# Optimization experiments

Hardware: AMD Instinct MI355X
Metric: run time of the kernel (lower is better)

Reference implementation:

```python
import jax, jax.numpy as jnp
import numpy as np

HEADS = 4

def _dwconv(x, w, pad):
    # depthwise conv, NCHW, kernel [C,1,k,k]
    return jax.lax.conv_general_dilated(
        x, w, window_strides=(1, 1), padding=((pad, pad), (pad, pad)),
        feature_group_count=x.shape[1],
        dimension_numbers=('NCHW', 'OIHW', 'NCHW'))

def _l2norm(t):
    # matches torch F.normalize(dim=-1, eps=1e-12)
    n = jnp.sqrt(jnp.sum(t * t, axis=-1, keepdims=True))
    return t / jnp.maximum(n, 1e-12)

def _reshape_attn(q, k, v, temp, if_box):
    b, c, hw0 = q.shape
    factor = HEADS
    ch = c // HEADS
    pad = (-hw0) % factor

    def prep(t):
        t = jnp.pad(t, ((0, 0), (0, 0), (0, pad)))
        hw = t.shape[-1] // factor
        if if_box:  # 'b (head c) (factor hw) -> b head (c factor) hw'
            t = t.reshape(b, HEADS, ch, factor, hw)
        else:       # 'b (head c) (hw factor) -> b head (c factor) hw'
            t = t.reshape(b, HEADS, ch, hw, factor).transpose(0, 1, 2, 4, 3)
        return t.reshape(b, HEADS, ch * factor, hw)

    qq, kk, vv = prep(q), prep(k), prep(v)
    qq, kk = _l2norm(qq), _l2norm(kk)
    attn = jnp.einsum('bhdn,bhen->bhde', qq, kk) * temp  # temp [heads,1,1]
    e = jnp.exp(attn)
    attn = e / (jnp.sum(e, axis=-1, keepdims=True) + 1.0)  # softmax_1
    o = jnp.einsum('bhde,bhen->bhdn', attn, vv)
    hw = o.shape[-1]
    if if_box:
        o = o.reshape(b, HEADS, ch, factor, hw).reshape(b, c, factor * hw)
    else:
        o = o.reshape(b, HEADS, ch, factor, hw).transpose(0, 1, 2, 4, 3).reshape(b, c, hw * factor)
    return o[:, :, :hw0]

def _conv1x1(x, w):
    return jnp.einsum('bchw,oc->bohw', x, w)

def _forward(x, temperature, w_qkv, w_dw3, w_dw5, w_dw7, w_fuse, b_fuse, w_proj):
    b, c, h, w = x.shape
    ch = c // 2
    # sort first half of channels along h then w
    xh = x[:, :ch]
    idx_h = jnp.argsort(xh, axis=-2)
    xs = jnp.take_along_axis(xh, idx_h, axis=-2)
    idx_w = jnp.argsort(xs, axis=-1)
    xs = jnp.take_along_axis(xs, idx_w, axis=-1)
    x = jnp.concatenate([xs, x[:, ch:]], axis=1)

    q = _conv1x1(x, w_qkv)  # [b,5c,h,w]
    cat = jnp.concatenate([_dwconv(q, w_dw3, 1), _dwconv(q, w_dw5, 2), _dwconv(q, w_dw7, 3)], axis=1)
    qkv = _conv1x1(cat, w_fuse) + b_fuse[None, :, None, None]
    q1, k1, q2, k2, v = jnp.split(qkv, 5, axis=1)

    hw = h * w
    vf = v.reshape(b, c, hw)
    idx = jnp.argsort(vf, axis=-1)
    vs = jnp.take_along_axis(vf, idx, axis=-1)
    gat = lambda t: jnp.take_along_axis(t.reshape(b, c, hw), idx, axis=-1)

    out1 = _reshape_attn(gat(q1), gat(k1), vs, temperature, True)
    out2 = _reshape_attn(gat(q2), gat(k2), vs, temperature, False)

    inv = jnp.argsort(idx, axis=-1)  # scatter(out, 2, idx, out) == unsort
    out1 = jnp.take_along_axis(out1, inv, axis=-1).reshape(b, c, h, w)
    out2 = jnp.take_along_axis(out2, inv, axis=-1).reshape(b, c, h, w)

    out = _conv1x1(out1 * out2, w_proj)
    r = out[:, :ch]
    r = jnp.take_along_axis(r, jnp.argsort(idx_w, axis=-1), axis=-1)
    r = jnp.take_along_axis(r, jnp.argsort(idx_h, axis=-2), axis=-2)
    return jnp.concatenate([r, out[:, ch:]], axis=1)

def setup_inputs() -> dict:
    key = jax.random.key(0)
    ks = jax.random.split(key, 8)
    b, c, h, w = 2, 64, 192, 192
    x = jax.random.normal(ks[0], (b, c, h, w), jnp.float32)
    temperature = jnp.ones((HEADS, 1, 1), jnp.float32)
    w_qkv = jax.random.normal(ks[1], (5 * c, c), jnp.float32) * 0.05
    w_dw3 = jax.random.normal(ks[2], (5 * c, 1, 3, 3), jnp.float32) * 0.1
    w_dw5 = jax.random.normal(ks[3], (5 * c, 1, 5, 5), jnp.float32) * 0.05
    w_dw7 = jax.random.normal(ks[4], (5 * c, 1, 7, 7), jnp.float32) * 0.03
    w_fuse = jax.random.normal(ks[5], (5 * c, 15 * c), jnp.float32) * 0.02
    b_fuse = jnp.zeros((5 * c,), jnp.float32)
    w_proj = jax.random.normal(ks[6], (c, c), jnp.float32) * 0.05
    return {'x': x, 'temperature': temperature, 'w_qkv': w_qkv, 'w_dw3': w_dw3,
            'w_dw5': w_dw5, 'w_dw7': w_dw7, 'w_fuse': w_fuse, 'b_fuse': b_fuse,
            'w_proj': w_proj}

def reference(x, temperature, w_qkv, w_dw3, w_dw5, w_dw7, w_fuse, b_fuse, w_proj):
    return _forward(x, temperature, w_qkv, w_dw3, w_dw5, w_dw7, w_fuse, b_fuse, w_proj)
```

## Files before the change

### kernel.cpp

```cpp
#include <hip/hip_runtime.h>
#include <stdint.h>
#include <stddef.h>

constexpr int IMH = 192;
constexpr int IMW = 192;
constexpr int HW  = 36864;
constexpr int BB  = 2;
constexpr int CC  = 64;
constexpr int CHF = 32;
constexpr int C5  = 320;
constexpr int NQ  = 9216;
constexpr int CROWS = 64;
constexpr int CHWN  = CROWS * IMW;
constexpr int NCHUNK = 32;
constexpr int CHN = HW / 4 / NCHUNK;
constexpr int NSEG = 12;
constexpr int SEGN = HW / NSEG;
constexpr int NBIN = 2048;

typedef float fx2 __attribute__((ext_vector_type(2)));
typedef float fx4 __attribute__((ext_vector_type(4)));
typedef _Float16 f16;
typedef _Float16 f16x8 __attribute__((ext_vector_type(8)));
typedef float f32x4 __attribute__((ext_vector_type(4)));

static __device__ __forceinline__ uint32_t f2s(float f) {
    uint32_t u = __float_as_uint(f);
    return (u & 0x80000000u) ? ~u : (u | 0x80000000u);
}
static __device__ __forceinline__ float s2f(uint32_t s) {
    uint32_t u = (s & 0x80000000u) ? (s & 0x7FFFFFFFu) : ~s;
    return __uint_as_float(u);
}

static __device__ void bitonic256(uint64_t* keys, int tid) {
    for (unsigned k = 2; k <= 256; k <<= 1) {
        for (unsigned j = k >> 1; j; j >>= 1) {
            __syncthreads();
            unsigned i = ((tid & ~(j - 1)) << 1) | (tid & (j - 1));
            unsigned p = i | j;
            bool up = ((i & k) == 0);
            uint64_t a = keys[i], b = keys[p];
            if ((a > b) == up) { keys[i] = b; keys[p] = a; }
        }
    }
    __syncthreads();
}

__global__ __launch_bounds__(128) void k_sort_h(const float* __restrict__ x, float* __restrict__ A,
                                                int* __restrict__ idx_h) {
    __shared__ uint64_t keys[256];
    int tid = threadIdx.x;
    int blk = blockIdx.x;
    int w = blk % IMW;
    int c = (blk / IMW) % CHF;
    int b = blk / (IMW * CHF);
    const float* col = x + ((size_t)(b * CC) + c) * HW + w;
    for (int i = tid; i < 256; i += 128)
        keys[i] = (i < IMH) ? ((((uint64_t)f2s(col[(size_t)i * IMW])) << 32) | (uint32_t)i) : ~0ull;
    bitonic256(keys, tid);
    float* ocol = A + ((size_t)(b * CC) + c) * HW + w;
    int* icol = idx_h + ((size_t)(b * CHF) + c) * HW + w;
    for (int i = tid; i < IMH; i += 128) {
        uint64_t k = keys[i];
        ocol[(size_t)i * IMW] = s2f((uint32_t)(k >> 32));
        icol[(size_t)i * IMW] = (int)(k & 0xFFFFFFFFull);
    }
}

__global__ __launch_bounds__(128) void k_sort_w(float* __restrict__ A, int* __restrict__ idx_w) {
    __shared__ uint64_t keys[256];
    int tid = threadIdx.x;
    int blk = blockIdx.x;
    int h = blk % IMH;
    int c = (blk / IMH) % CHF;
    int b = blk / (IMH * CHF);
    float* row = A + ((size_t)(b * CC) + c) * HW + (size_t)h * IMW;
    for (int i = tid; i < 256; i += 128)
        keys[i] = (i < IMW) ? ((((uint64_t)f2s(row[i])) << 32) | (uint32_t)i) : ~0ull;
    bitonic256(keys, tid);
    int* irow = idx_w + ((size_t)(b * CHF) + c) * HW + (size_t)h * IMW;
    for (int i = tid; i < IMW; i += 128) {
        uint64_t k = keys[i];
        row[i] = s2f((uint32_t)(k >> 32));
        irow[i] = (int)(k & 0xFFFFFFFFull);
    }
}

__global__ __launch_bounds__(256) void k_gemm_q(const float* __restrict__ wq, const float* __restrict__ A,
                                                const float* __restrict__ x, float* __restrict__ q) {
    __shared__ float Wt[64][68];
    __shared__ float Xt[64][68];
    int tid = threadIdx.x;
    int n0 = blockIdx.x * 64, m0 = blockIdx.y * 64, b = blockIdx.z;
    for (int l = 0; l < 16; ++l) {
        int idx = l * 256 + tid;
        int cc = idx & 63, m = idx >> 6;
        Wt[cc][m] = wq[(size_t)(m0 + m) * 64 + cc];
    }
    for (int l = 0; l < 16; ++l) {
        int idx = l * 256 + tid;
        int n = idx & 63, cc = idx >> 6;
        const float* sp = (cc < CHF) ? A : x;
        Xt[cc][n] = sp[((size_t)(b * CC) + cc) * HW + n0 + n];
    }
    __syncthreads();
    int ty = tid >> 4, tx = tid & 15;
    float acc[4][4] = {};
    for (int cc = 0; cc < 64; ++cc) {
        float4 av = *(const float4*)&Wt[cc][ty * 4];
        float4 bv = *(const float4*)&Xt[cc][tx * 4];
        float aa[4] = {av.x, av.y, av.z, av.w};
        float bb[4] = {bv.x, bv.y, bv.z, bv.w};
        #pragma unroll
        for (int i = 0; i < 4; ++i)
            #pragma unroll
            for (int j = 0; j < 4; ++j)
                acc[i][j] = fmaf(aa[i], bb[j], acc[i][j]);
    }
    for (int i = 0; i < 4; ++i) {
        float4 o;
        o.x = acc[i][0]; o.y = acc[i][1]; o.z = acc[i][2]; o.w = acc[i][3];
        *(float4*)&q[((size_t)(b * C5) + m0 + ty * 4 + i) * HW + n0 + tx * 4] = o;
    }
}

template <int KS>
__global__ __launch_bounds__(256) void k_dwconv(const float* __restrict__ q, const float* __restrict__ wd,
                                                float* __restrict__ slice, int r0) {
    constexpr int PAD = KS / 2;
    constexpr int EXT = 32 + 2 * PAD;
    __shared__ float tile[EXT][EXT];
    int tid = threadIdx.x;
    int b = blockIdx.z, c = blockIdx.y;
    int t = blockIdx.x;
    int ty0 = r0 + (t / 6) * 32, tx0 = (t % 6) * 32;
    const float* src = q + ((size_t)(b * C5) + c) * HW;
    for (int i = tid; i < EXT * EXT; i += 256) {
        int iy = i / EXT, ix = i % EXT;
        int gy = ty0 + iy - PAD, gx = tx0 + ix - PAD;
        float v = 0.f;
        if (gy >= 0 && gy < IMH && gx >= 0 && gx < IMW) v = src[gy * IMW + gx];
        tile[iy][ix] = v;
    }
    __syncthreads();
    float wreg[KS * KS];
    #pragma unroll
    for (int i = 0; i < KS * KS; ++i) wreg[i] = wd[(size_t)c * KS * KS + i];
    float* dst = slice + ((size_t)(b * C5) + c) * CHWN;
    #pragma unroll
    for (int k = 0; k < 4; ++k) {
        int pix = k * 256 + tid;
        int py = pix >> 5, px = pix & 31;
        float acc = 0.f;
        #pragma unroll
        for (int ky = 0; ky < KS; ++ky)
            #pragma unroll
            for (int kx = 0; kx < KS; ++kx)
                acc = fmaf(tile[py + ky][px + kx], wreg[ky * KS + kx], acc);
        dst[(ty0 - r0 + py) * IMW + tx0 + px] = acc;
    }
}

__global__ __launch_bounds__(256) void k_gemm_fuse(const float* __restrict__ wf,
                                                   const float* __restrict__ slice, const float* __restrict__ bias,
                                                   float* __restrict__ qkv, int g, int r0) {
    __shared__ f16 Ah[64][40];
    __shared__ f16 Al[64][40];
    int tid = threadIdx.x;
    int n0 = blockIdx.x * 128, m0 = blockIdx.y * 64, b = blockIdx.z;
    int lane = tid & 63, wv = tid >> 6;
    int l15 = lane & 15, lg = lane >> 4;
    int nwave = n0 + wv * 32;
    int sm = tid >> 2, skr = (tid & 3) * 8;
    int gk = g * 320;
    f32x4 acc[4][2];
    #pragma unroll
    for (int i = 0; i < 4; ++i)
        #pragma unroll
        for (int j = 0; j < 2; ++j)
            acc[i][j] = (f32x4){0.f, 0.f, 0.f, 0.f};

    const float* xcol = slice + (size_t)(b * C5) * CHWN + nwave + l15;
    const float* wrow = wf + (size_t)(m0 + sm) * 960 + gk + skr;

    for (int k0 = 0; k0 < 320; k0 += 32) {
        if (k0) __syncthreads();
        {
            float4 w0 = *(const float4*)(wrow + k0);
            float4 w1 = *(const float4*)(wrow + k0 + 4);
            float wvv[8] = {w0.x, w0.y, w0.z, w0.w, w1.x, w1.y, w1.z, w1.w};
            f16x8 hv, lv;
            #pragma unroll
            for (int j = 0; j < 8; ++j) {
                f16 h = (f16)wvv[j];
                hv[j] = h;
                lv[j] = (f16)(wvv[j] - (float)h);
            }
            *(f16x8*)&Ah[sm][skr] = hv;
            *(f16x8*)&Al[sm][skr] = lv;
        }
        float xv[2][8];
        #pragma unroll
        for (int fn = 0; fn < 2; ++fn)
            #pragma unroll
            for (int j = 0; j < 8; ++j)
                xv[fn][j] = xcol[(size_t)(k0 + lg * 8 + j) * CHWN + fn * 16];
        __syncthreads();
        f16x8 bh[2], bl[2];
        #pragma unroll
        for (int fn = 0; fn < 2; ++fn)
            #pragma unroll
            for (int j = 0; j < 8; ++j) {
                float v = xv[fn][j];
                f16 h = (f16)v;
                bh[fn][j] = h;
                bl[fn][j] = (f16)(v - (float)h);
            }
        #pragma unroll
        for (int fm = 0; fm < 4; ++fm) {
            f16x8 ah = *(const f16x8*)&Ah[fm * 16 + l15][lg * 8];
            f16x8 al = *(const f16x8*)&Al[fm * 16 + l15][lg * 8];
            #pragma unroll
            for (int fn = 0; fn < 2; ++fn) {
                acc[fm][fn] = __builtin_amdgcn_mfma_f32_16x16x32_f16(ah, bh[fn], acc[fm][fn], 0, 0, 0);
                acc[fm][fn] = __builtin_amdgcn_mfma_f32_16x16x32_f16(ah, bl[fn], acc[fm][fn], 0, 0, 0);
                acc[fm][fn] = __builtin_amdgcn_mfma_f32_16x16x32_f16(al, bh[fn], acc[fm][fn], 0, 0, 0);
            }
        }
    }

    #pragma unroll
    for (int fm = 0; fm < 4; ++fm) {
        #pragma unroll
        for (int r = 0; r < 4; ++r) {
            int m = m0 + fm * 16 + lg * 4 + r;
            size_t base = ((size_t)(b * C5) + m) * HW + (size_t)r0 * IMW;
            if (g == 0) {
                float bv = bias[m];
                #pragma unroll
                for (int fn = 0; fn < 2; ++fn)
                    qkv[base + nwave + fn * 16 + l15] = acc[fm][fn][r] + bv;
            } else {
                #pragma unroll
                for (int fn = 0; fn < 2; ++fn)
                    qkv[base + nwave + fn * 16 + l15] += acc[fm][fn][r];
            }
        }
    }
}

template <int FIRST>
__global__ __launch_bounds__(256) void k_rcount(const uint64_t* __restrict__ in, const float* __restrict__ qkvv,
                                                uint32_t* __restrict__ cntG, int shift) {
    __shared__ uint32_t hist[NBIN];
    int t = threadIdx.x;
    int seg = blockIdx.x, row = blockIdx.y;
    #pragma unroll
    for (int k = 0; k < NBIN / 256; ++k) hist[k * 256 + t] = 0;
    __syncthreads();
    if (FIRST) {
        int bb = row >> 6, c = row & 63;
        const float* srcf = qkvv + ((size_t)(bb * C5) + 256 + c) * HW + (size_t)seg * SEGN;
        #pragma unroll
        for (int i = 0; i < SEGN / 256; ++i) {
            unsigned d = f2s(srcf[i * 256 + t]) & (NBIN - 1);
            atomicAdd(&hist[d], 1u);
        }
    } else {
        const uint64_t* src = in + (size_t)row * HW + (size_t)seg * SEGN;
        #pragma unroll
        for (int i = 0; i < SEGN / 256; ++i) {
            unsigned d = (unsigned)(src[i * 256 + t] >> shift) & (NBIN - 1);
            atomicAdd(&hist[d], 1u);
        }
    }
    __syncthreads();
    uint32_t* dstc = cntG + ((size_t)row * NSEG + seg) * NBIN;
    #pragma unroll
    for (int k = 0; k < NBIN / 256; ++k) dstc[k * 256 + t] = hist[k * 256 + t];
}

__global__ __launch_bounds__(256) void k_rscan(uint32_t* __restrict__ cntG) {
    __shared__ uint32_t tot[NBIN];
    __shared__ uint32_t gsum[256];
    __shared__ uint32_t gbase[256];
    int t = threadIdx.x;
    int row = blockIdx.x;
    uint32_t* base = cntG + (size_t)row * NSEG * NBIN;
    uint32_t loc = 0;
    #pragma unroll
    for (int k = 0; k < NBIN / 256; ++k) {
        int bn = t * (NBIN / 256) + k;
        uint32_t s = 0;
        for (int sg = 0; sg < NSEG; ++sg) s += base[sg * NBIN + bn];
        tot[bn] = s;
        loc += s;
    }
    gsum[t] = loc;
    __syncthreads();
    if (t == 0) {
        uint32_t acc = 0;
        for (int i = 0; i < 256; ++i) { uint32_t v = gsum[i]; gbase[i] = acc; acc += v; }
    }
    __syncthreads();
    uint32_t run = gbase[t];
    #pragma unroll
    for (int k = 0; k < NBIN / 256; ++k) {
        int bn = t * (NBIN / 256) + k;
        uint32_t tv = tot[bn];
        uint32_t r2 = run;
        for (int sg = 0; sg < NSEG; ++sg) {
            uint32_t cv = base[sg * NBIN + bn];
            base[sg * NBIN + bn] = r2;
            r2 += cv;
        }
        run += tv;
    }
}

template <int MODE>
__global__ __launch_bounds__(256) void k_rscatter(const uint64_t* __restrict__ in, const float* __restrict__ qkvv,
                                                  uint64_t* __restrict__ out, float* __restrict__ vso,
                                                  int* __restrict__ idxo, int* __restrict__ inv0o,
                                                  int* __restrict__ inv1o, const uint32_t* __restrict__ cntG,
                                                  int shift) {
    __shared__ uint16_t wcnt[4][NBIN];
    __shared__ uint32_t runbase[NBIN];
    int t = threadIdx.x;
    int w = t >> 6, lane = t & 63;
    int seg = blockIdx.x, row = blockIdx.y;
    const uint32_t* cbase = cntG + ((size_t)row * NSEG + seg) * NBIN;
    #pragma unroll
    for (int k = 0; k < NBIN / 256; ++k) runbase[k * 256 + t] = cbase[k * 256 + t];
    for (int i = 0; i < SEGN / 256; ++i) {
        __syncthreads();
        #pragma unroll
        for (int k = 0; k < NBIN / 256; ++k)
            ((uint64_t*)wcnt)[k * 256 + t] = 0;
        __syncthreads();
        uint64_t kv;
        if (MODE == 1) {
            int bb = row >> 6, c = row & 63;
            const float* srcf = qkvv + ((size_t)(bb * C5) + 256 + c) * HW + (size_t)seg * SEGN;
            kv = (((uint64_t)f2s(srcf[i * 256 + t])) << 32) | (uint32_t)(seg * SEGN + i * 256 + t);
        } else {
            const uint64_t* src = in + (size_t)row * HW + (size_t)seg * SEGN;
            kv = src[i * 256 + t];
        }
        unsigned d = (unsigned)(kv >> shift) & (NBIN - 1);
        uint64_t peers = ~0ull;
        #pragma unroll
        for (int bit = 0; bit < 11; ++bit) {
            uint64_t bm = __ballot((d >> bit) & 1u);
            peers &= ((d >> bit) & 1u) ? bm : ~bm;
        }
        unsigned lanerank = (unsigned)__popcll(peers & ((1ull << lane) - 1ull));
        unsigned wtotal = (unsigned)__popcll(peers);
        if (lanerank == 0) wcnt[w][d] = (uint16_t)wtotal;
        __syncthreads();
        unsigned wpre = 0;
        #pragma unroll
        for (int ww = 0; ww < 4; ++ww) {
            unsigned cv = wcnt[ww][d];
            if (ww < w) wpre += cv;
        }
        unsigned pos = runbase[d] + wpre + lanerank;
        if (MODE == 2) {
            int j = (int)(kv & 0xFFFFFFFFull);
            vso[(size_t)row * HW + pos] = s2f((uint32_t)(kv >> 32));
            idxo[(size_t)row * HW + pos] = j;
            int bb = row >> 6, c = row & 63;
            int* ip = (bb ? inv1o : inv0o) + (size_t)c * HW;
            ip[j] = (int)pos;
        } else {
            out[(size_t)row * HW + pos] = kv;
        }
        __syncthreads();
        #pragma unroll
        for (int k = 0; k < NBIN / 256; ++k) {
            int bn = k * 256 + t;
            runbase[bn] += (uint32_t)wcnt[0][bn] + wcnt[1][bn] + wcnt[2][bn] + wcnt[3][bn];
        }
    }
}

__global__ __launch_bounds__(1024) void k_scatter4(const int* __restrict__ inv0, const int* __restrict__ inv1,
                                                   const float* __restrict__ qkv, float* __restrict__ g4) {
    int i = blockIdx.x;
    int row = (i & 7) * 16 + ((i >> 3) & 15);
    int jh = i >> 7;
    int b = row >> 6, cg = row & 63;
    const int* irow = (b ? inv1 : inv0) + (size_t)cg * HW + jh * (HW / 2);
    size_t S4 = (size_t)BB * CC * HW;
    int tid = threadIdx.x;
    int2 pinv[9];
    #pragma unroll
    for (int s = 0; s < 9; ++s)
        pinv[s] = *(const int2*)&irow[s * 2048 + tid * 2];
    for (int ph = 0; ph < 4; ++ph) {
        const float* src = qkv + ((size_t)(b * C5) + ph * 64 + cg) * HW + jh * (HW / 2);
        float* dst = g4 + (size_t)ph * S4 + (size_t)row * HW;
        #pragma unroll 3
        for (int s = 0; s < 9; ++s) {
            fx2 v = __builtin_nontemporal_load((const fx2*)&src[s * 2048 + tid * 2]);
            dst[pinv[s].x] = v.x;
            dst[pinv[s].y] = v.y;
        }
        __syncthreads();
    }
}

__global__ __launch_bounds__(256) void k_attn_qk(const float* __restrict__ g4,
                                                 float* __restrict__ partS, float* __restrict__ partN) {
    __shared__ float Qs[16][68];
    __shared__ float Ks[16][68];
    __shared__ float nqs[4][64];
    __shared__ float nks[4][64];
    int tid = threadIdx.x;
    int ychunk = blockIdx.x;
    int z = blockIdx.y;
    int vi = z & 1, hh = (z >> 1) & 3, b = z >> 3;
    size_t S4 = (size_t)BB * CC * HW;
    const float* Q = g4 + (vi ? 2 * S4 : (size_t)0);
    const float* Kp = g4 + (vi ? 3 * S4 : S4);
    int ty = tid >> 4, tx = tid & 15;
    float acc[4][4] = {};
    float nq = 0.f, nk = 0.f;
    int d0 = tid & 63, kset = tid >> 6;
    int nbase0 = ychunk * CHN;
    for (int it = 0; it < CHN / 16; ++it) {
        int nb0 = nbase0 + it * 16;
        __syncthreads();
        #pragma unroll
        for (int l = 0; l < 4; ++l) {
            int idx = l * 256 + tid;
            int d = idx >> 4, kk = idx & 15;
            int n = nb0 + kk;
            int cch = hh * 16 + (d >> 2), f = d & 3;
            size_t off = ((size_t)(b * CC) + cch) * HW + (vi ? (size_t)(n * 4 + f) : (size_t)(f * NQ + n));
            Qs[kk][d] = Q[off];
            Ks[kk][d] = Kp[off];
        }
        __syncthreads();
        #pragma unroll
        for (int kk = 0; kk < 16; ++kk) {
            float4 av = *(const float4*)&Qs[kk][ty * 4];
            float4 bv = *(const float4*)&Ks[kk][tx * 4];
            float aa[4] = {av.x, av.y, av.z, av.w};
            float bb[4] = {bv.x, bv.y, bv.z, bv.w};
            #pragma unroll
            for (int i = 0; i < 4; ++i)
                #pragma unroll
                for (int j = 0; j < 4; ++j)
                    acc[i][j] = fmaf(aa[i], bb[j], acc[i][j]);
        }
        #pragma unroll
        for (int kk2 = 0; kk2 < 4; ++kk2) {
            float qv = Qs[kset * 4 + kk2][d0];
            float kv = Ks[kset * 4 + kk2][d0];
            nq = fmaf(qv, qv, nq);
            nk = fmaf(kv, kv, nk);
        }
    }
    size_t sb = ((size_t)z * NCHUNK + ychunk) * 4096;
    #pragma unroll
    for (int i = 0; i < 4; ++i)
        #pragma unroll
        for (int j = 0; j < 4; ++j)
            partS[sb + (size_t)(ty * 4 + i) * 64 + tx * 4 + j] = acc[i][j];
    nqs[kset][d0] = nq;
    nks[kset][d0] = nk;
    __syncthreads();
    if (tid < 64) {
        float sq = nqs[0][tid] + nqs[1][tid] + nqs[2][tid] + nqs[3][tid];
        float sk = nks[0][tid] + nks[1][tid] + nks[2][tid] + nks[3][tid];
        size_t nb2 = ((size_t)z * NCHUNK + ychunk) * 128;
        partN[nb2 + tid] = sq;
        partN[nb2 + 64 + tid] = sk;
    }
}

__global__ __launch_bounds__(256) void k_attn_softmax(const float* __restrict__ partS,
                                                      const float* __restrict__ partN,
                                                      const float* __restrict__ temp, float* __restrict__ attnT) {
    __shared__ float nqv[64], nkv[64];
    __shared__ float pbuf[64][65];
    __shared__ float rred[64][4];
    __shared__ float rsum[64];
    int tid = threadIdx.x;
    int z = blockIdx.x;
    int hh = (z >> 1) & 3;
    if (tid < 128) {
        float s = 0.f;
        for (int ch = 0; ch < NCHUNK; ++ch) s += partN[((size_t)z * NCHUNK + ch) * 128 + tid];
        float nv = fmaxf(sqrtf(s), 1e-12f);
        if (tid < 64) nqv[tid] = nv; else nkv[tid - 64] = nv;
    }
    __syncthreads();
    float tf = temp[hh];
    int d = tid >> 2, qq = tid & 3;
    float psum = 0.f;
    for (int e = qq * 16; e < qq * 16 + 16; ++e) {
        float s = 0.f;
        for (int ch = 0; ch < NCHUNK; ++ch) s += partS[((size_t)z * NCHUNK + ch) * 4096 + (size_t)d * 64 + e];
        float p = expf(tf * s / (nqv[d] * nkv[e]));
        pbuf[d][e] = p;
        psum += p;
    }
    rred[d][qq] = psum;
    __syncthreads();
    if (tid < 64) rsum[tid] = rred[tid][0] + rred[tid][1] + rred[tid][2] + rred[tid][3] + 1.0f;
    __syncthreads();
    for (int e = qq * 16; e < qq * 16 + 16; ++e)
        attnT[(size_t)z * 4096 + (size_t)e * 64 + d] = pbuf[d][e] / rsum[d];
}

__global__ __launch_bounds__(256) void k_attn_av(const float* __restrict__ attnT, const float* __restrict__ vs,
                                                 float* __restrict__ O1, float* __restrict__ O2) {
    __shared__ float at_s[4096];
    int tid = threadIdx.x;
    int z = blockIdx.y;
    int vi = z & 1, hh = (z >> 1) & 3, b = z >> 3;
    for (int l = 0; l < 16; ++l) at_s[l * 256 + tid] = attnT[(size_t)z * 4096 + l * 256 + tid];
    __syncthreads();
    int n = blockIdx.x * 256 + tid;
    float acc[64];
    #pragma unroll
    for (int d = 0; d < 64; ++d) acc[d] = 0.f;
    for (int e = 0; e < 64; ++e) {
        int cch = hh * 16 + (e >> 2), f = e & 3;
        size_t p = vi ? (size_t)(n * 4 + f) : (size_t)(f * NQ + n);
        float vv = vs[((size_t)(b * CC) + cch) * HW + p];
        const float* ar = &at_s[e * 64];
        #pragma unroll
        for (int d4 = 0; d4 < 16; ++d4) {
            float4 a4 = *(const float4*)&ar[d4 * 4];
            acc[d4 * 4 + 0] = fmaf(a4.x, vv, acc[d4 * 4 + 0]);
            acc[d4 * 4 + 1] = fmaf(a4.y, vv, acc[d4 * 4 + 1]);
            acc[d4 * 4 + 2] = fmaf(a4.z, vv, acc[d4 * 4 + 2]);
            acc[d4 * 4 + 3] = fmaf(a4.w, vv, acc[d4 * 4 + 3]);
        }
    }
    float* Ob = vi ? O2 : O1;
    #pragma unroll
    for (int d = 0; d < 64; ++d) {
        int cch = hh * 16 + (d >> 2), f = d & 3;
        size_t p = vi ? (size_t)(n * 4 + f) : (size_t)(f * NQ + n);
        Ob[((size_t)(b * CC) + cch) * HW + p] = acc[d];
    }
}

__global__ void k_prod_scatter(const float* __restrict__ O1, const float* __restrict__ O2,
                               const int* __restrict__ idxv, float* __restrict__ pu) {
    int j = blockIdx.x * 256 + threadIdx.x;
    int row = blockIdx.y;
    size_t o = (size_t)row * HW + j;
    int p = idxv[o];
    pu[(size_t)row * HW + p] = O1[o] * O2[o];
}

__global__ __launch_bounds__(256) void k_gemm_proj(const float* __restrict__ wp, const float* __restrict__ pu,
                                                   float* __restrict__ op) {
    __shared__ float wt[2048];
    int tid = threadIdx.x;
    int mh = blockIdx.y, b = blockIdx.z;
    for (int l = 0; l < 8; ++l) {
        int i = l * 256 + tid;
        int mm = i >> 6, c = i & 63;
        wt[c * 32 + mm] = wp[(size_t)(mh * 32 + mm) * 64 + c];
    }
    __syncthreads();
    int n = blockIdx.x * 256 + tid;
    float acc[32];
    #pragma unroll
    for (int m = 0; m < 32; ++m) acc[m] = 0.f;
    const float* src = pu + (size_t)(b * CC) * HW + n;
    for (int c = 0; c < 64; ++c) {
        float xv = src[(size_t)c * HW];
        const float* wr = &wt[c * 32];
        #pragma unroll
        for (int m4 = 0; m4 < 8; ++m4) {
            float4 w4 = *(const float4*)&wr[m4 * 4];
            acc[m4 * 4 + 0] = fmaf(w4.x, xv, acc[m4 * 4 + 0]);
            acc[m4 * 4 + 1] = fmaf(w4.y, xv, acc[m4 * 4 + 1]);
            acc[m4 * 4 + 2] = fmaf(w4.z, xv, acc[m4 * 4 + 2]);
            acc[m4 * 4 + 3] = fmaf(w4.w, xv, acc[m4 * 4 + 3]);
        }
    }
    float* dst = op + ((size_t)(b * CC) + mh * 32) * HW + n;
    for (int m = 0; m < 32; ++m) dst[(size_t)m * HW] = acc[m];
}

__global__ void k_final(const float* __restrict__ op, const int* __restrict__ idx_h,
                        const int* __restrict__ idx_w, float* __restrict__ out) {
    int i = blockIdx.x * 256 + threadIdx.x;
    int p = i % HW;
    int c = (i / HW) % CC;
    int b = i / (HW * CC);
    float v = op[i];
    if (c < CHF) {
        int h = p / IMW, w = p % IMW;
        size_t ib = ((size_t)(b * CHF) + c) * HW;
        int W0 = idx_w[ib + h * IMW + w];
        int H0 = idx_h[ib + h * IMW + W0];
        out[((size_t)(b * CC) + c) * HW + H0 * IMW + W0] = v;
    } else {
        out[i] = v;
    }
}

extern "C" void kernel_launch(void* const* d_in, const int* in_sizes, int n_in,
                              void* d_out, int out_size, void* d_ws, size_t ws_size,
                              hipStream_t stream) {
    (void)in_sizes; (void)n_in; (void)out_size; (void)ws_size;
    const float* x    = (const float*)d_in[0];
    const float* temp = (const float*)d_in[1];
    const float* wq   = (const float*)d_in[2];
    const float* wd3  = (const float*)d_in[3];
    const float* wd5  = (const float*)d_in[4];
    const float* wd7  = (const float*)d_in[5];
    const float* wf   = (const float*)d_in[6];
    const float* bf   = (const float*)d_in[7];
    const float* wp   = (const float*)d_in[8];
    float* out = (float*)d_out;
    float* ws = (float*)d_ws;

    int*      idx_h = (int*)(ws + 0);
    int*      idx_w = (int*)(ws + 2359296);
    float*    A     = ws + 4718592;
    float*    slice = ws + 4718592;
    float*    q     = ws + 12582912;
    float*    qkv   = ws + 36175872;
    int*      idxv  = (int*)(ws + 4718592);
    uint32_t* cntG  = (uint32_t*)(ws + 9437184);
    uint64_t* keyA  = (uint64_t*)(ws + 12582912);
    uint64_t* keyB  = (uint64_t*)(ws + 22020096);
    float*    vs    = ws + 31457280;
    int*      inv0  = (int*)(ws + 45613056);
    int*      inv1  = (int*)(ws + 57409536);
    float*    g4    = ws + 12582912;
    float*    O1    = ws + 36175872;
    float*    O2    = ws + 40894464;
    float*    pu    = ws + 45613056;
    float*    op    = ws + 50331648;
    float*    partS = ws + 55050240;
    float*    partN = ws + 57147392;
    float*    attnT = ws + 57212928;

    k_sort_h<<<12288, 128, 0, stream>>>(x, A, idx_h);
    k_sort_w<<<12288, 128, 0, stream>>>(A, idx_w);
    k_gemm_q<<<dim3(576, 5, 2), 256, 0, stream>>>(wq, A, x, q);

    for (int g = 0; g < 3; ++g) {
        for (int chunk = 0; chunk < 3; ++chunk) {
            int r0 = chunk * CROWS;
            if (g == 0)      k_dwconv<3><<<dim3(12, 320, 2), 256, 0, stream>>>(q, wd3, slice, r0);
            else if (g == 1) k_dwconv<5><<<dim3(12, 320, 2), 256, 0, stream>>>(q, wd5, slice, r0);
            else             k_dwconv<7><<<dim3(12, 320, 2), 256, 0, stream>>>(q, wd7, slice, r0);
            k_gemm_fuse<<<dim3(96, 5, 2), 256, 0, stream>>>(wf, slice, bf, qkv, g, r0);
        }
    }

    k_rcount<1><<<dim3(NSEG, 128), 256, 0, stream>>>(nullptr, qkv, cntG, 32);
    k_rscan<<<128, 256, 0, stream>>>(cntG);
    k_rscatter<1><<<dim3(NSEG, 128), 256, 0, stream>>>(nullptr, qkv, keyB, nullptr, nullptr, nullptr, nullptr, cntG, 32);
    k_rcount<0><<<dim3(NSEG, 128), 256, 0, stream>>>(keyB, nullptr, cntG, 43);
    k_rscan<<<128, 256, 0, stream>>>(cntG);
    k_rscatter<0><<<dim3(NSEG, 128), 256, 0, stream>>>(keyB, nullptr, keyA, nullptr, nullptr, nullptr, nullptr, cntG, 43);
    k_rcount<0><<<dim3(NSEG, 128), 256, 0, stream>>>(keyA, nullptr, cntG, 54);
    k_rscan<<<128, 256, 0, stream>>>(cntG);
    k_rscatter<2><<<dim3(NSEG, 128), 256, 0, stream>>>(keyA, nullptr, nullptr, vs, idxv, inv0, inv1, cntG, 54);

    k_scatter4<<<256, 1024, 0, stream>>>(inv0, inv1, qkv, g4);

    k_attn_qk<<<dim3(NCHUNK, 16), 256, 0, stream>>>(g4, partS, partN);
    k_attn_softmax<<<16, 256, 0, stream>>>(partS, partN, temp, attnT);
    k_attn_av<<<dim3(36, 16), 256, 0, stream>>>(attnT, vs, O1, O2);

    k_prod_scatter<<<dim3(144, 128), 256, 0, stream>>>(O1, O2, idxv, pu);
    k_gemm_proj<<<dim3(144, 2, 2), 256, 0, stream>>>(wp, pu, op);
    k_final<<<18432, 256, 0, stream>>>(op, idx_h, idx_w, out);
}
```

Baseline: 1.337 ms.

## Interleave q/k outputs and replace inverse-permutation scatter with a gather

The fuse GEMM now writes the four q/k projections interleaved per pixel into one buffer (qkvI) and v into a separate buffer (qkvV). The last radix scatter no longer builds inverse-permutation arrays. The old per-projection scatter kernel becomes a single gather that reads one float4 per sorted index and writes the four planes with coalesced nontemporal stores. This removes random scattered writes and the inverse-index traffic, at the cost of strided 4-way interleaved stores in the GEMM epilogue and random float4 reads in the gather.

```diff
diff --git a/kernel.cpp b/kernel.cpp
--- a/kernel.cpp
+++ b/kernel.cpp
@@ -164,11 +164,12 @@
 
 __global__ __launch_bounds__(256) void k_gemm_fuse(const float* __restrict__ wf,
                                                    const float* __restrict__ slice, const float* __restrict__ bias,
-                                                   float* __restrict__ qkv, int g, int r0) {
+                                                   float* __restrict__ qkvI, float* __restrict__ qkvV,
+                                                   int g, int r0) {
     __shared__ f16 Ah[64][40];
     __shared__ f16 Al[64][40];
     int tid = threadIdx.x;
-    int n0 = blockIdx.x * 128, m0 = blockIdx.y * 64, b = blockIdx.z;
+    int n0 = blockIdx.x * 128, py = blockIdx.y, m0 = py * 64, b = blockIdx.z;
     int lane = tid & 63, wv = tid >> 6;
     int l15 = lane & 15, lg = lane >> 4;
     int nwave = n0 + wv * 32;
@@ -235,16 +236,32 @@
         #pragma unroll
         for (int r = 0; r < 4; ++r) {
             int m = m0 + fm * 16 + lg * 4 + r;
-            size_t base = ((size_t)(b * C5) + m) * HW + (size_t)r0 * IMW;
-            if (g == 0) {
-                float bv = bias[m];
-                #pragma unroll
-                for (int fn = 0; fn < 2; ++fn)
-                    qkv[base + nwave + fn * 16 + l15] = acc[fm][fn][r] + bv;
+            int cg = m & 63;
+            size_t colb = (size_t)r0 * IMW + nwave + l15;
+            if (py < 4) {
+                float* bp = qkvI + ((size_t)(b * CC + cg) * HW) * 4 + py;
+                if (g == 0) {
+                    float bv = bias[m];
+                    #pragma unroll
+                    for (int fn = 0; fn < 2; ++fn)
+                        bp[(colb + fn * 16) * 4] = acc[fm][fn][r] + bv;
+                } else {
+                    #pragma unroll
+                    for (int fn = 0; fn < 2; ++fn)
+                        bp[(colb + fn * 16) * 4] += acc[fm][fn][r];
+                }
             } else {
-                #pragma unroll
-                for (int fn = 0; fn < 2; ++fn)
-                    qkv[base + nwave + fn * 16 + l15] += acc[fm][fn][r];
+                float* bp = qkvV + (size_t)(b * CC + cg) * HW;
+                if (g == 0) {
+                    float bv = bias[m];
+                    #pragma unroll
+                    for (int fn = 0; fn < 2; ++fn)
+                        bp[colb + fn * 16] = acc[fm][fn][r] + bv;
+                } else {
+                    #pragma unroll
+                    for (int fn = 0; fn < 2; ++fn)
+                        bp[colb + fn * 16] += acc[fm][fn][r];
+                }
             }
         }
     }
@@ -260,8 +277,7 @@
     for (int k = 0; k < NBIN / 256; ++k) hist[k * 256 + t] = 0;
     __syncthreads();
     if (FIRST) {
-        int bb = row >> 6, c = row & 63;
-        const float* srcf = qkvv + ((size_t)(bb * C5) + 256 + c) * HW + (size_t)seg * SEGN;
+        const float* srcf = qkvv + (size_t)row * HW + (size_t)seg * SEGN;
         #pragma unroll
         for (int i = 0; i < SEGN / 256; ++i) {
             unsigned d = f2s(srcf[i * 256 + t]) & (NBIN - 1);
@@ -322,8 +338,7 @@
 template <int MODE>
 __global__ __launch_bounds__(256) void k_rscatter(const uint64_t* __restrict__ in, const float* __restrict__ qkvv,
                                                   uint64_t* __restrict__ out, float* __restrict__ vso,
-                                                  int* __restrict__ idxo, int* __restrict__ inv0o,
-                                                  int* __restrict__ inv1o, const uint32_t* __restrict__ cntG,
+                                                  int* __restrict__ idxo, const uint32_t* __restrict__ cntG,
                                                   int shift) {
     __shared__ uint16_t wcnt[4][NBIN];
     __shared__ uint32_t runbase[NBIN];
@@ -341,8 +356,7 @@
         __syncthreads();
         uint64_t kv;
         if (MODE == 1) {
-            int bb = row >> 6, c = row & 63;
-            const float* srcf = qkvv + ((size_t)(bb * C5) + 256 + c) * HW + (size_t)seg * SEGN;
+            const float* srcf = qkvv + (size_t)row * HW + (size_t)seg * SEGN;
             kv = (((uint64_t)f2s(srcf[i * 256 + t])) << 32) | (uint32_t)(seg * SEGN + i * 256 + t);
         } else {
             const uint64_t* src = in + (size_t)row * HW + (size_t)seg * SEGN;
@@ -367,12 +381,8 @@
         }
         unsigned pos = runbase[d] + wpre + lanerank;
         if (MODE == 2) {
-            int j = (int)(kv & 0xFFFFFFFFull);
             vso[(size_t)row * HW + pos] = s2f((uint32_t)(kv >> 32));
-            idxo[(size_t)row * HW + pos] = j;
-            int bb = row >> 6, c = row & 63;
-            int* ip = (bb ? inv1o : inv0o) + (size_t)c * HW;
-            ip[j] = (int)pos;
+            idxo[(size_t)row * HW + pos] = (int)(kv & 0xFFFFFFFFull);
         } else {
             out[(size_t)row * HW + pos] = kv;
         }
@@ -385,29 +395,34 @@
     }
 }
 
-__global__ __launch_bounds__(1024) void k_scatter4(const int* __restrict__ inv0, const int* __restrict__ inv1,
-                                                   const float* __restrict__ qkv, float* __restrict__ g4) {
+__global__ __launch_bounds__(1024) void k_gather4(const int* __restrict__ idxv, const float* __restrict__ qkvI,
+                                                  float* __restrict__ g4) {
     int i = blockIdx.x;
     int row = (i & 7) * 16 + ((i >> 3) & 15);
     int jh = i >> 7;
-    int b = row >> 6, cg = row & 63;
-    const int* irow = (b ? inv1 : inv0) + (size_t)cg * HW + jh * (HW / 2);
+    const int* irow = idxv + (size_t)row * HW + jh * (HW / 2);
     size_t S4 = (size_t)BB * CC * HW;
     int tid = threadIdx.x;
-    int2 pinv[9];
-    #pragma unroll
-    for (int s = 0; s < 9; ++s)
-        pinv[s] = *(const int2*)&irow[s * 2048 + tid * 2];
-    for (int ph = 0; ph < 4; ++ph) {
-        const float* src = qkv + ((size_t)(b * C5) + ph * 64 + cg) * HW + jh * (HW / 2);
-        float* dst = g4 + (size_t)ph * S4 + (size_t)row * HW;
-        #pragma unroll 3
-        for (int s = 0; s < 9; ++s) {
-            fx2 v = __builtin_nontemporal_load((const fx2*)&src[s * 2048 + tid * 2]);
-            dst[pinv[s].x] = v.x;
-            dst[pinv[s].y] = v.y;
-        }
-        __syncthreads();
+    const fx4* src = (const fx4*)(qkvI + (size_t)row * HW * 4);
+    size_t dbase = (size_t)row * HW + jh * (HW / 2);
+    float* d0 = g4 + dbase;
+    float* d1 = d0 + S4;
+    float* d2 = d0 + 2 * S4;
+    float* d3 = d0 + 3 * S4;
+    #pragma unroll 3
+    for (int s = 0; s < 9; ++s) {
+        int j = s * 2048 + tid * 2;
+        int2 p = *(const int2*)&irow[j];
+        fx4 a = src[p.x];
+        fx4 b4 = src[p.y];
+        fx2 w0 = {a.x, b4.x};
+        fx2 w1 = {a.y, b4.y};
+        fx2 w2 = {a.z, b4.z};
+        fx2 w3 = {a.w, b4.w};
+        __builtin_nontemporal_store(w0, (fx2*)&d0[j]);
+        __builtin_nontemporal_store(w1, (fx2*)&d1[j]);
+        __builtin_nontemporal_store(w2, (fx2*)&d2[j]);
+        __builtin_nontemporal_store(w3, (fx2*)&d3[j]);
     }
 }
 
@@ -631,14 +646,13 @@
     float*    A     = ws + 4718592;
     float*    slice = ws + 4718592;
     float*    q     = ws + 12582912;
-    float*    qkv   = ws + 36175872;
+    float*    qkvI  = ws + 36175872;
+    float*    qkvV  = ws + 55050240;
     int*      idxv  = (int*)(ws + 4718592);
     uint32_t* cntG  = (uint32_t*)(ws + 9437184);
     uint64_t* keyA  = (uint64_t*)(ws + 12582912);
     uint64_t* keyB  = (uint64_t*)(ws + 22020096);
     float*    vs    = ws + 31457280;
-    int*      inv0  = (int*)(ws + 45613056);
-    int*      inv1  = (int*)(ws + 57409536);
     float*    g4    = ws + 12582912;
     float*    O1    = ws + 36175872;
     float*    O2    = ws + 40894464;
@@ -658,21 +672,21 @@
             if (g == 0)      k_dwconv<3><<<dim3(12, 320, 2), 256, 0, stream>>>(q, wd3, slice, r0);
             else if (g == 1) k_dwconv<5><<<dim3(12, 320, 2), 256, 0, stream>>>(q, wd5, slice, r0);
             else             k_dwconv<7><<<dim3(12, 320, 2), 256, 0, stream>>>(q, wd7, slice, r0);
-            k_gemm_fuse<<<dim3(96, 5, 2), 256, 0, stream>>>(wf, slice, bf, qkv, g, r0);
-        }
-    }
-
-    k_rcount<1><<<dim3(NSEG, 128), 256, 0, stream>>>(nullptr, qkv, cntG, 32);
+            k_gemm_fuse<<<dim3(96, 5, 2), 256, 0, stream>>>(wf, slice, bf, qkvI, qkvV, g, r0);
+        }
+    }
+
+    k_rcount<1><<<dim3(NSEG, 128), 256, 0, stream>>>(nullptr, qkvV, cntG, 32);
     k_rscan<<<128, 256, 0, stream>>>(cntG);
-    k_rscatter<1><<<dim3(NSEG, 128), 256, 0, stream>>>(nullptr, qkv, keyB, nullptr, nullptr, nullptr, nullptr, cntG, 32);
+    k_rscatter<1><<<dim3(NSEG, 128), 256, 0, stream>>>(nullptr, qkvV, keyB, nullptr, nullptr, cntG, 32);
     k_rcount<0><<<dim3(NSEG, 128), 256, 0, stream>>>(keyB, nullptr, cntG, 43);
     k_rscan<<<128, 256, 0, stream>>>(cntG);
-    k_rscatter<0><<<dim3(NSEG, 128), 256, 0, stream>>>(keyB, nullptr, keyA, nullptr, nullptr, nullptr, nullptr, cntG, 43);
+    k_rscatter<0><<<dim3(NSEG, 128), 256, 0, stream>>>(keyB, nullptr, keyA, nullptr, nullptr, cntG, 43);
     k_rcount<0><<<dim3(NSEG, 128), 256, 0, stream>>>(keyA, nullptr, cntG, 54);
     k_rscan<<<128, 256, 0, stream>>>(cntG);
-    k_rscatter<2><<<dim3(NSEG, 128), 256, 0, stream>>>(keyA, nullptr, nullptr, vs, idxv, inv0, inv1, cntG, 54);
-
-    k_scatter4<<<256, 1024, 0, stream>>>(inv0, inv1, qkv, g4);
+    k_rscatter<2><<<dim3(NSEG, 128), 256, 0, stream>>>(keyA, nullptr, nullptr, vs, idxv, cntG, 54);
+
+    k_gather4<<<256, 1024, 0, stream>>>(idxv, qkvI, g4);
 
     k_attn_qk<<<dim3(NCHUNK, 16), 256, 0, stream>>>(g4, partS, partN);
     k_attn_softmax<<<16, 256, 0, stream>>>(partS, partN, temp, attnT);
```

Result: faster. 1.207 ms (-9.7%).
